# Optimization experiments

Hardware: AMD Instinct MI355X
Metric: run time of the kernel (lower is better)

Reference implementation:

```python
import jax, jax.numpy as jnp
import numpy as np

TEMPERATURE = 1.0
MIN_DISP = 0.1


def setup_inputs() -> dict:
    key = jax.random.key(0)
    k1, = jax.random.split(key, 1)
    B, V, C, H, W = 4, 2, 128, 128, 512
    feat = jax.random.normal(k1, (B, V, C, H, W), dtype=jnp.float32)
    # normalized intrinsics (fx < 50 triggers normalized_intri branch)
    K = jnp.array([[0.8, 0.0, 0.5], [0.0, 0.8, 0.5], [0.0, 0.0, 1.0]], dtype=jnp.float32)
    intri = jnp.broadcast_to(K, (B, V, 3, 3))
    # extrinsics: left = identity, right = identity translated by baseline 0.1 in x
    eye = jnp.eye(4, dtype=jnp.float32)
    lext = jnp.broadcast_to(eye, (B, 4, 4))
    rext = eye.at[0, 3].set(0.1)
    rext = jnp.broadcast_to(rext, (B, 4, 4))
    extri = jnp.stack([lext, rext], axis=1)
    near = jnp.full((B, V), 0.1, dtype=jnp.float32)
    far = jnp.full((B, V), 10.0, dtype=jnp.float32)
    return {"feat": feat, "extri": extri, "intri": intri, "near": near, "far": far}


def reference(feat, extri, intri, near, far):
    B, V, C, H, W = feat.shape
    lfeat, rfeat = feat[:, 0], feat[:, 1]          # (B,C,H,W)
    lintri = intri[:, 0]
    lextri, rextri = extri[:, 0], extri[:, 1]
    lfar = far[:, 0]

    # dot-product cost volume, groups G=1: (B,1,H,W1,W2)
    vol = jnp.einsum('bchi,bchj->bhij', lfeat, rfeat) / np.sqrt(C)
    vol = vol[:, None]

    # triangular geometry mask (left image first -> tril), applied AFTER softmax
    mask = jnp.tril(jnp.ones((W, W), dtype=vol.dtype))
    idx = jnp.arange(W, dtype=vol.dtype)
    prob = jax.nn.softmax(vol / TEMPERATURE, axis=-1) * mask

    # soft-argmax correspondence and confidence
    corresp = jnp.sum(prob * idx, axis=-1)         # (B,1,H,W)
    conf = jnp.max(prob, axis=-1)                  # (B,1,H,W)

    # correspondence -> normalized disparity -> depth
    disp = jnp.abs(corresp - idx) / W
    disp = jnp.maximum(disp, MIN_DISP)
    fx = lintri[:, 0, 0][:, None, None, None]
    baseline = jnp.linalg.norm(lextri[:, :3, 3] - rextri[:, :3, 3], axis=-1)
    depth = fx * baseline[:, None, None, None] / disp

    # depth_type == 'norm_depth'
    depth_conversed = depth / lfar[:, None, None, None]

    out = jnp.concatenate((depth_conversed, conf), axis=1)[:, None]  # (B,1,2,H,W)
    return out
```

## Files before the change

### kernel.cpp

```cpp
#include <hip/hip_runtime.h>

typedef _Float16 f16x8 __attribute__((ext_vector_type(8)));
typedef _Float16 f16x4 __attribute__((ext_vector_type(4)));
typedef float    f32x4 __attribute__((ext_vector_type(4)));

#define C_DIM 128
#define H_DIM 128
#define W_DIM 512
#define CH_STRIDE 65536
#define V_STRIDE  8388608
#define SJ 32
#define NSTRIP 16
#define ROW_H 136

__global__ __launch_bounds__(512, 2) void costvol_kernel(
    const float* __restrict__ feat,
    const float* __restrict__ extri,
    const float* __restrict__ intri,
    const float* __restrict__ farp,
    float* __restrict__ out)
{
    __shared__ _Float16 Bs[2][SJ][ROW_H];

    const int tid  = threadIdx.x;
    const int wave = tid >> 6;
    const int lane = tid & 63;
    const int l15  = lane & 15;
    const int l4   = lane >> 4;

    const int bh = blockIdx.x;
    const int b  = bh >> 7;
    const int h  = bh & 127;

    const float* lbase = feat + (size_t)(b * 2) * V_STRIDE + (size_t)h * W_DIM;
    const float* rbase = lbase + V_STRIDE;

    const int jj = tid & 31;
    const int c0 = (tid >> 5) * 4;

    float br[8];
    {
        const float* bp = rbase + jj;
        #pragma unroll
        for (int d = 0; d < 4; ++d) {
            br[d]     = bp[(size_t)(c0 + d) * CH_STRIDE];
            br[4 + d] = bp[(size_t)(c0 + d + 64) * CH_STRIDE];
        }
    }
    __builtin_amdgcn_sched_barrier(0);

    f16x8 a[4][4];
    const float kScale = 0.08838834764831845f;
    #pragma unroll
    for (int ks = 0; ks < 4; ++ks) {
        #pragma unroll
        for (int fi = 0; fi < 4; ++fi) {
            const float* p = lbase + (size_t)(ks * 32 + l4 * 8) * CH_STRIDE
                             + (size_t)(wave * 64 + fi * 16 + l15);
            f16x8 f;
            #pragma unroll
            for (int e = 0; e < 8; ++e)
                f[e] = (_Float16)(p[(size_t)e * CH_STRIDE] * kScale);
            a[fi][ks] = f;
        }
        __builtin_amdgcn_sched_barrier(0);
    }

    {
        f16x4 w0, w1;
        #pragma unroll
        for (int d = 0; d < 4; ++d) { w0[d] = (_Float16)br[d]; w1[d] = (_Float16)br[4 + d]; }
        *(f16x4*)&Bs[0][jj][c0]      = w0;
        *(f16x4*)&Bs[0][jj][c0 + 64] = w1;
    }
    __syncthreads();

    float Zp[16], Mp[16], Wp[16];
    #pragma unroll
    for (int s2 = 0; s2 < 16; ++s2) { Zp[s2] = 0.f; Mp[s2] = 0.f; Wp[s2] = 0.f; }

    int buf = 0;
    for (int s = 0; s < NSTRIP; ++s) {
        if (s + 1 < NSTRIP) {
            const float* bp = rbase + (size_t)((s + 1) * SJ + jj);
            #pragma unroll
            for (int d = 0; d < 4; ++d) {
                br[d]     = bp[(size_t)(c0 + d) * CH_STRIDE];
                br[4 + d] = bp[(size_t)(c0 + d + 64) * CH_STRIDE];
            }
        }
        __builtin_amdgcn_sched_barrier(0);

        f32x4 acc[4][2];
        #pragma unroll
        for (int fi = 0; fi < 4; ++fi) {
            acc[fi][0] = (f32x4){0.f, 0.f, 0.f, 0.f};
            acc[fi][1] = (f32x4){0.f, 0.f, 0.f, 0.f};
        }
        #pragma unroll
        for (int ks = 0; ks < 4; ++ks) {
            f16x8 b0 = *(const f16x8*)&Bs[buf][l15][ks * 32 + l4 * 8];
            f16x8 b1 = *(const f16x8*)&Bs[buf][16 + l15][ks * 32 + l4 * 8];
            #pragma unroll
            for (int fi = 0; fi < 4; ++fi) {
                acc[fi][0] = __builtin_amdgcn_mfma_f32_16x16x32_f16(a[fi][ks], b0, acc[fi][0], 0, 0, 0);
                acc[fi][1] = __builtin_amdgcn_mfma_f32_16x16x32_f16(a[fi][ks], b1, acc[fi][1], 0, 0, 0);
            }
        }

        const int jbase = s * SJ;
        #pragma unroll
        for (int fi = 0; fi < 4; ++fi) {
            const int ti0 = wave * 64 + fi * 16;
            #pragma unroll
            for (int fj = 0; fj < 2; ++fj) {
                const int tj = jbase + fj * 16;
                const float jf = (float)(tj + l15);
                if (tj + 15 <= ti0) {
                    #pragma unroll
                    for (int r = 0; r < 4; ++r) {
                        const int sl = fi * 4 + r;
                        float e = __expf(acc[fi][fj][r]);
                        Zp[sl] += e;
                        Mp[sl] = fmaxf(Mp[sl], e);
                        Wp[sl] += jf * e;
                    }
                } else if (tj > ti0 + 15) {
                    #pragma unroll
                    for (int r = 0; r < 4; ++r) {
                        float e = __expf(acc[fi][fj][r]);
                        Zp[fi * 4 + r] += e;
                    }
                } else {
                    #pragma unroll
                    for (int r = 0; r < 4; ++r) {
                        const int sl = fi * 4 + r;
                        float e = __expf(acc[fi][fj][r]);
                        Zp[sl] += e;
                        const int irow = ti0 + l4 * 4 + r;
                        float em = ((tj + l15) <= irow) ? e : 0.f;
                        Mp[sl] = fmaxf(Mp[sl], em);
                        Wp[sl] += jf * em;
                    }
                }
            }
        }

        if (s + 1 < NSTRIP) {
            f16x4 w0, w1;
            #pragma unroll
            for (int d = 0; d < 4; ++d) { w0[d] = (_Float16)br[d]; w1[d] = (_Float16)br[4 + d]; }
            *(f16x4*)&Bs[buf ^ 1][jj][c0]      = w0;
            *(f16x4*)&Bs[buf ^ 1][jj][c0 + 64] = w1;
        }
        __syncthreads();
        buf ^= 1;
    }

    #pragma unroll
    for (int m = 1; m <= 8; m <<= 1) {
        #pragma unroll
        for (int sl = 0; sl < 16; ++sl) {
            Zp[sl] += __shfl_xor(Zp[sl], m, 64);
            Wp[sl] += __shfl_xor(Wp[sl], m, 64);
            Mp[sl] = fmaxf(Mp[sl], __shfl_xor(Mp[sl], m, 64));
        }
    }

    if (l15 == 0) {
        const float fx = intri[b * 18];
        const float dx = extri[b * 32 + 3]  - extri[b * 32 + 19];
        const float dy = extri[b * 32 + 7]  - extri[b * 32 + 23];
        const float dz = extri[b * 32 + 11] - extri[b * 32 + 27];
        const float bl = sqrtf(dx * dx + dy * dy + dz * dz);
        const float lfar = farp[b * 2];
        const float kd = fx * bl / lfar;
        #pragma unroll
        for (int sl = 0; sl < 16; ++sl) {
            const int fi = sl >> 2, r = sl & 3;
            const int irow = wave * 64 + fi * 16 + l4 * 4 + r;
            const float Z = Zp[sl];
            const float conf = Mp[sl] / Z;
            const float corr = Wp[sl] / Z;
            float disp = fabsf(corr - (float)irow) * (1.0f / 512.0f);
            disp = fmaxf(disp, 0.1f);
            out[(size_t)(b * 2 + 0) * CH_STRIDE + h * W_DIM + irow] = kd / disp;
            out[(size_t)(b * 2 + 1) * CH_STRIDE + h * W_DIM + irow] = conf;
        }
    }
}

extern "C" void kernel_launch(void* const* d_in, const int* in_sizes, int n_in,
                              void* d_out, int out_size, void* d_ws, size_t ws_size,
                              hipStream_t stream) {
    const float* feat  = (const float*)d_in[0];
    const float* extri = (const float*)d_in[1];
    const float* intri = (const float*)d_in[2];
    const float* farp  = (const float*)d_in[4];
    float* out = (float*)d_out;
    costvol_kernel<<<dim3(512), dim3(512), 0, stream>>>(feat, extri, intri, farp, out);
}
```

Baseline: 90.92 us.

## Prefetch right-image strips two ahead with dual register buffers and MFMA priority

Restructures the strip loop to keep two register prefetch buffers in flight, so global loads for strip s+2 and s+3 overlap compute on earlier strips. Each thread now loads 8 consecutive channels and does one f16x8 LDS store instead of two f16x4 stores. It raises wave priority around the MFMA block and changes launch bounds to ask for 4 blocks per CU. The extra registers for the second buffer plus the tighter occupancy target risk spills or lower achieved occupancy.

```diff
diff --git a/kernel.cpp b/kernel.cpp
--- a/kernel.cpp
+++ b/kernel.cpp
@@ -1,7 +1,6 @@
 #include <hip/hip_runtime.h>
 
 typedef _Float16 f16x8 __attribute__((ext_vector_type(8)));
-typedef _Float16 f16x4 __attribute__((ext_vector_type(4)));
 typedef float    f32x4 __attribute__((ext_vector_type(4)));
 
 #define C_DIM 128
@@ -13,7 +12,7 @@
 #define NSTRIP 16
 #define ROW_H 136
 
-__global__ __launch_bounds__(512, 2) void costvol_kernel(
+__global__ __launch_bounds__(512, 4) void costvol_kernel(
     const float* __restrict__ feat,
     const float* __restrict__ extri,
     const float* __restrict__ intri,
@@ -36,17 +35,26 @@
     const float* rbase = lbase + V_STRIDE;
 
     const int jj = tid & 31;
-    const int c0 = (tid >> 5) * 4;
-
-    float br[8];
-    {
-        const float* bp = rbase + jj;
-        #pragma unroll
-        for (int d = 0; d < 4; ++d) {
-            br[d]     = bp[(size_t)(c0 + d) * CH_STRIDE];
-            br[4 + d] = bp[(size_t)(c0 + d + 64) * CH_STRIDE];
-        }
-    }
+    const int c0 = (tid >> 5) * 8;
+
+    float brA[8], brB[8];
+
+#define ISSUE(br, s) do {                                                   \
+    const float* bp_ = rbase + (size_t)((s) * SJ + jj);                     \
+    _Pragma("unroll")                                                       \
+    for (int d_ = 0; d_ < 8; ++d_)                                          \
+        (br)[d_] = bp_[(size_t)(c0 + d_) * CH_STRIDE];                      \
+} while (0)
+
+#define STAGE(br, bf) do {                                                  \
+    f16x8 w_;                                                               \
+    _Pragma("unroll")                                                       \
+    for (int d_ = 0; d_ < 8; ++d_) w_[d_] = (_Float16)(br)[d_];             \
+    *(f16x8*)&Bs[bf][jj][c0] = w_;                                          \
+} while (0)
+
+    ISSUE(brA, 0);
+    ISSUE(brB, 1);
     __builtin_amdgcn_sched_barrier(0);
 
     f16x8 a[4][4];
@@ -66,95 +74,84 @@
         __builtin_amdgcn_sched_barrier(0);
     }
 
-    {
-        f16x4 w0, w1;
-        #pragma unroll
-        for (int d = 0; d < 4; ++d) { w0[d] = (_Float16)br[d]; w1[d] = (_Float16)br[4 + d]; }
-        *(f16x4*)&Bs[0][jj][c0]      = w0;
-        *(f16x4*)&Bs[0][jj][c0 + 64] = w1;
-    }
+    STAGE(brA, 0);
     __syncthreads();
 
     float Zp[16], Mp[16], Wp[16];
     #pragma unroll
     for (int s2 = 0; s2 < 16; ++s2) { Zp[s2] = 0.f; Mp[s2] = 0.f; Wp[s2] = 0.f; }
 
-    int buf = 0;
-    for (int s = 0; s < NSTRIP; ++s) {
-        if (s + 1 < NSTRIP) {
-            const float* bp = rbase + (size_t)((s + 1) * SJ + jj);
-            #pragma unroll
-            for (int d = 0; d < 4; ++d) {
-                br[d]     = bp[(size_t)(c0 + d) * CH_STRIDE];
-                br[4 + d] = bp[(size_t)(c0 + d + 64) * CH_STRIDE];
-            }
-        }
+#define COMPUTE(bf, s) do {                                                  \
+    f32x4 acc[4][2];                                                         \
+    _Pragma("unroll")                                                        \
+    for (int fi = 0; fi < 4; ++fi) {                                         \
+        acc[fi][0] = (f32x4){0.f, 0.f, 0.f, 0.f};                            \
+        acc[fi][1] = (f32x4){0.f, 0.f, 0.f, 0.f};                            \
+    }                                                                        \
+    __builtin_amdgcn_s_setprio(1);                                           \
+    _Pragma("unroll")                                                        \
+    for (int ks = 0; ks < 4; ++ks) {                                         \
+        f16x8 b0 = *(const f16x8*)&Bs[bf][l15][ks * 32 + l4 * 8];            \
+        f16x8 b1 = *(const f16x8*)&Bs[bf][16 + l15][ks * 32 + l4 * 8];       \
+        _Pragma("unroll")                                                    \
+        for (int fi = 0; fi < 4; ++fi) {                                     \
+            acc[fi][0] = __builtin_amdgcn_mfma_f32_16x16x32_f16(a[fi][ks], b0, acc[fi][0], 0, 0, 0); \
+            acc[fi][1] = __builtin_amdgcn_mfma_f32_16x16x32_f16(a[fi][ks], b1, acc[fi][1], 0, 0, 0); \
+        }                                                                    \
+    }                                                                        \
+    __builtin_amdgcn_s_setprio(0);                                           \
+    const int jbase_ = (s) * SJ;                                             \
+    _Pragma("unroll")                                                        \
+    for (int fi = 0; fi < 4; ++fi) {                                         \
+        const int ti0 = wave * 64 + fi * 16;                                 \
+        _Pragma("unroll")                                                    \
+        for (int fj = 0; fj < 2; ++fj) {                                     \
+            const int tj = jbase_ + fj * 16;                                 \
+            const float jf = (float)(tj + l15);                              \
+            if (tj + 15 <= ti0) {                     \
+                _Pragma("unroll")                                            \
+                for (int r = 0; r < 4; ++r) {                                \
+                    const int sl = fi * 4 + r;                               \
+                    float e = __expf(acc[fi][fj][r]);                        \
+                    Zp[sl] += e;                                             \
+                    Mp[sl] = fmaxf(Mp[sl], e);                               \
+                    Wp[sl] += jf * e;                                        \
+                }                                                            \
+            } else if (tj > ti0 + 15) {                    \
+                _Pragma("unroll")                                            \
+                for (int r = 0; r < 4; ++r) {                                \
+                    float e = __expf(acc[fi][fj][r]);                        \
+                    Zp[fi * 4 + r] += e;                                     \
+                }                                                            \
+            } else {                                      \
+                _Pragma("unroll")                                            \
+                for (int r = 0; r < 4; ++r) {                                \
+                    const int sl = fi * 4 + r;                               \
+                    float e = __expf(acc[fi][fj][r]);                        \
+                    Zp[sl] += e;                                             \
+                    const int irow = ti0 + l4 * 4 + r;                       \
+                    float em = ((tj + l15) <= irow) ? e : 0.f;               \
+                    Mp[sl] = fmaxf(Mp[sl], em);                              \
+                    Wp[sl] += jf * em;                                       \
+                }                                                            \
+            }                                                                \
+        }                                                                    \
+    }                                                                        \
+} while (0)
+
+    #pragma unroll 1
+    for (int s = 0; s < NSTRIP; s += 2) {
+        if (s + 2 < NSTRIP) ISSUE(brA, s + 2);
         __builtin_amdgcn_sched_barrier(0);
-
-        f32x4 acc[4][2];
-        #pragma unroll
-        for (int fi = 0; fi < 4; ++fi) {
-            acc[fi][0] = (f32x4){0.f, 0.f, 0.f, 0.f};
-            acc[fi][1] = (f32x4){0.f, 0.f, 0.f, 0.f};
-        }
-        #pragma unroll
-        for (int ks = 0; ks < 4; ++ks) {
-            f16x8 b0 = *(const f16x8*)&Bs[buf][l15][ks * 32 + l4 * 8];
-            f16x8 b1 = *(const f16x8*)&Bs[buf][16 + l15][ks * 32 + l4 * 8];
-            #pragma unroll
-            for (int fi = 0; fi < 4; ++fi) {
-                acc[fi][0] = __builtin_amdgcn_mfma_f32_16x16x32_f16(a[fi][ks], b0, acc[fi][0], 0, 0, 0);
-                acc[fi][1] = __builtin_amdgcn_mfma_f32_16x16x32_f16(a[fi][ks], b1, acc[fi][1], 0, 0, 0);
-            }
-        }
-
-        const int jbase = s * SJ;
-        #pragma unroll
-        for (int fi = 0; fi < 4; ++fi) {
-            const int ti0 = wave * 64 + fi * 16;
-            #pragma unroll
-            for (int fj = 0; fj < 2; ++fj) {
-                const int tj = jbase + fj * 16;
-                const float jf = (float)(tj + l15);
-                if (tj + 15 <= ti0) {
-                    #pragma unroll
-                    for (int r = 0; r < 4; ++r) {
-                        const int sl = fi * 4 + r;
-                        float e = __expf(acc[fi][fj][r]);
-                        Zp[sl] += e;
-                        Mp[sl] = fmaxf(Mp[sl], e);
-                        Wp[sl] += jf * e;
-                    }
-                } else if (tj > ti0 + 15) {
-                    #pragma unroll
-                    for (int r = 0; r < 4; ++r) {
-                        float e = __expf(acc[fi][fj][r]);
-                        Zp[fi * 4 + r] += e;
-                    }
-                } else {
-                    #pragma unroll
-                    for (int r = 0; r < 4; ++r) {
-                        const int sl = fi * 4 + r;
-                        float e = __expf(acc[fi][fj][r]);
-                        Zp[sl] += e;
-                        const int irow = ti0 + l4 * 4 + r;
-                        float em = ((tj + l15) <= irow) ? e : 0.f;
-                        Mp[sl] = fmaxf(Mp[sl], em);
-                        Wp[sl] += jf * em;
-                    }
-                }
-            }
-        }
-
-        if (s + 1 < NSTRIP) {
-            f16x4 w0, w1;
-            #pragma unroll
-            for (int d = 0; d < 4; ++d) { w0[d] = (_Float16)br[d]; w1[d] = (_Float16)br[4 + d]; }
-            *(f16x4*)&Bs[buf ^ 1][jj][c0]      = w0;
-            *(f16x4*)&Bs[buf ^ 1][jj][c0 + 64] = w1;
-        }
+        COMPUTE(0, s);
+        STAGE(brB, 1);
         __syncthreads();
-        buf ^= 1;
+
+        if (s + 3 < NSTRIP) ISSUE(brB, s + 3);
+        __builtin_amdgcn_sched_barrier(0);
+        COMPUTE(1, s + 1);
+        if (s + 2 < NSTRIP) STAGE(brA, 0);
+        __syncthreads();
     }
 
     #pragma unroll
@@ -188,6 +185,9 @@
             out[(size_t)(b * 2 + 1) * CH_STRIDE + h * W_DIM + irow] = conf;
         }
     }
+#undef ISSUE
+#undef STAGE
+#undef COMPUTE
 }
 
 extern "C" void kernel_launch(void* const* d_in, const int* in_sizes, int n_in,
```

After: 328.8 us. 262% more time.

## Stage full right row in LDS, use 1024-thread blocks and exp2

Applied to the files above, without the earlier changes.

The kernel now loads the entire right-image row (512 columns × 128 channels, fp16) into LDS in one pass instead of double-buffering 32-column strips. This removes the per-strip barriers and the pipelined global prefetch. Blocks grow to 16 waves, each owning 32 rows, with the MFMA phase at raised wave priority. The log2(e) factor is folded into the A scaling so exp2f can replace expf. In exchange, the single upfront load is no longer overlapped with compute, and the larger LDS footprint (~139KB) may cap occupancy at one block per CU despite the launch-bounds hint.

```diff
diff --git a/kernel.cpp b/kernel.cpp
--- a/kernel.cpp
+++ b/kernel.cpp
@@ -1,7 +1,6 @@
 #include <hip/hip_runtime.h>
 
 typedef _Float16 f16x8 __attribute__((ext_vector_type(8)));
-typedef _Float16 f16x4 __attribute__((ext_vector_type(4)));
 typedef float    f32x4 __attribute__((ext_vector_type(4)));
 
 #define C_DIM 128
@@ -9,18 +8,16 @@
 #define W_DIM 512
 #define CH_STRIDE 65536
 #define V_STRIDE  8388608
-#define SJ 32
-#define NSTRIP 16
 #define ROW_H 136
 
-__global__ __launch_bounds__(512, 2) void costvol_kernel(
+__global__ __launch_bounds__(1024, 4) void costvol_kernel(
     const float* __restrict__ feat,
     const float* __restrict__ extri,
     const float* __restrict__ intri,
     const float* __restrict__ farp,
     float* __restrict__ out)
 {
-    __shared__ _Float16 Bs[2][SJ][ROW_H];
+    __shared__ _Float16 Bs[W_DIM][ROW_H];
 
     const int tid  = threadIdx.x;
     const int wave = tid >> 6;
@@ -31,136 +28,100 @@
     const int bh = blockIdx.x;
     const int b  = bh >> 7;
     const int h  = bh & 127;
+    const int rowbase = wave * 32;
 
     const float* lbase = feat + (size_t)(b * 2) * V_STRIDE + (size_t)h * W_DIM;
     const float* rbase = lbase + V_STRIDE;
 
-    const int jj = tid & 31;
-    const int c0 = (tid >> 5) * 4;
-
-    float br[8];
-    {
-        const float* bp = rbase + jj;
-        #pragma unroll
-        for (int d = 0; d < 4; ++d) {
-            br[d]     = bp[(size_t)(c0 + d) * CH_STRIDE];
-            br[4 + d] = bp[(size_t)(c0 + d + 64) * CH_STRIDE];
-        }
-    }
-    __builtin_amdgcn_sched_barrier(0);
-
-    f16x8 a[4][4];
-    const float kScale = 0.08838834764831845f;
+    f16x8 a[2][4];
+    const float kScale = 0.08838834764831845f * 1.44269504088896340f;
     #pragma unroll
     for (int ks = 0; ks < 4; ++ks) {
         #pragma unroll
-        for (int fi = 0; fi < 4; ++fi) {
+        for (int fi = 0; fi < 2; ++fi) {
             const float* p = lbase + (size_t)(ks * 32 + l4 * 8) * CH_STRIDE
-                             + (size_t)(wave * 64 + fi * 16 + l15);
+                             + (size_t)(rowbase + fi * 16 + l15);
             f16x8 f;
             #pragma unroll
             for (int e = 0; e < 8; ++e)
                 f[e] = (_Float16)(p[(size_t)e * CH_STRIDE] * kScale);
             a[fi][ks] = f;
         }
-        __builtin_amdgcn_sched_barrier(0);
     }
 
     {
-        f16x4 w0, w1;
+        const int j      = tid & 511;
+        const int chbase = (tid >> 9) << 6;
         #pragma unroll
-        for (int d = 0; d < 4; ++d) { w0[d] = (_Float16)br[d]; w1[d] = (_Float16)br[4 + d]; }
-        *(f16x4*)&Bs[0][jj][c0]      = w0;
-        *(f16x4*)&Bs[0][jj][c0 + 64] = w1;
+        for (int cb = 0; cb < 8; ++cb) {
+            const int c0 = chbase + cb * 8;
+            const float* bp = rbase + (size_t)c0 * CH_STRIDE + j;
+            f16x8 w;
+            #pragma unroll
+            for (int e = 0; e < 8; ++e)
+                w[e] = (_Float16)bp[(size_t)e * CH_STRIDE];
+            *(f16x8*)&Bs[j][c0] = w;
+        }
     }
     __syncthreads();
 
-    float Zp[16], Mp[16], Wp[16];
+    float Zp[8], Mp[8], Wp[8];
     #pragma unroll
-    for (int s2 = 0; s2 < 16; ++s2) { Zp[s2] = 0.f; Mp[s2] = 0.f; Wp[s2] = 0.f; }
+    for (int s2 = 0; s2 < 8; ++s2) { Zp[s2] = 0.f; Mp[s2] = 0.f; Wp[s2] = 0.f; }
 
-    int buf = 0;
-    for (int s = 0; s < NSTRIP; ++s) {
-        if (s + 1 < NSTRIP) {
-            const float* bp = rbase + (size_t)((s + 1) * SJ + jj);
-            #pragma unroll
-            for (int d = 0; d < 4; ++d) {
-                br[d]     = bp[(size_t)(c0 + d) * CH_STRIDE];
-                br[4 + d] = bp[(size_t)(c0 + d + 64) * CH_STRIDE];
-            }
-        }
-        __builtin_amdgcn_sched_barrier(0);
-
-        f32x4 acc[4][2];
-        #pragma unroll
-        for (int fi = 0; fi < 4; ++fi) {
-            acc[fi][0] = (f32x4){0.f, 0.f, 0.f, 0.f};
-            acc[fi][1] = (f32x4){0.f, 0.f, 0.f, 0.f};
-        }
+    #pragma unroll 1
+    for (int jt = 0; jt < 32; ++jt) {
+        f32x4 acc[2];
+        acc[0] = (f32x4){0.f, 0.f, 0.f, 0.f};
+        acc[1] = (f32x4){0.f, 0.f, 0.f, 0.f};
+        __builtin_amdgcn_s_setprio(1);
         #pragma unroll
         for (int ks = 0; ks < 4; ++ks) {
-            f16x8 b0 = *(const f16x8*)&Bs[buf][l15][ks * 32 + l4 * 8];
-            f16x8 b1 = *(const f16x8*)&Bs[buf][16 + l15][ks * 32 + l4 * 8];
-            #pragma unroll
-            for (int fi = 0; fi < 4; ++fi) {
-                acc[fi][0] = __builtin_amdgcn_mfma_f32_16x16x32_f16(a[fi][ks], b0, acc[fi][0], 0, 0, 0);
-                acc[fi][1] = __builtin_amdgcn_mfma_f32_16x16x32_f16(a[fi][ks], b1, acc[fi][1], 0, 0, 0);
-            }
+            f16x8 bf = *(const f16x8*)&Bs[jt * 16 + l15][ks * 32 + l4 * 8];
+            acc[0] = __builtin_amdgcn_mfma_f32_16x16x32_f16(a[0][ks], bf, acc[0], 0, 0, 0);
+            acc[1] = __builtin_amdgcn_mfma_f32_16x16x32_f16(a[1][ks], bf, acc[1], 0, 0, 0);
         }
+        __builtin_amdgcn_s_setprio(0);
 
-        const int jbase = s * SJ;
+        const int tj = jt * 16;
+        const float jf = (float)(tj + l15);
         #pragma unroll
-        for (int fi = 0; fi < 4; ++fi) {
-            const int ti0 = wave * 64 + fi * 16;
-            #pragma unroll
-            for (int fj = 0; fj < 2; ++fj) {
-                const int tj = jbase + fj * 16;
-                const float jf = (float)(tj + l15);
-                if (tj + 15 <= ti0) {
-                    #pragma unroll
-                    for (int r = 0; r < 4; ++r) {
-                        const int sl = fi * 4 + r;
-                        float e = __expf(acc[fi][fj][r]);
-                        Zp[sl] += e;
-                        Mp[sl] = fmaxf(Mp[sl], e);
-                        Wp[sl] += jf * e;
-                    }
-                } else if (tj > ti0 + 15) {
-                    #pragma unroll
-                    for (int r = 0; r < 4; ++r) {
-                        float e = __expf(acc[fi][fj][r]);
-                        Zp[fi * 4 + r] += e;
-                    }
-                } else {
-                    #pragma unroll
-                    for (int r = 0; r < 4; ++r) {
-                        const int sl = fi * 4 + r;
-                        float e = __expf(acc[fi][fj][r]);
-                        Zp[sl] += e;
-                        const int irow = ti0 + l4 * 4 + r;
-                        float em = ((tj + l15) <= irow) ? e : 0.f;
-                        Mp[sl] = fmaxf(Mp[sl], em);
-                        Wp[sl] += jf * em;
-                    }
+        for (int fi = 0; fi < 2; ++fi) {
+            const int ti0 = rowbase + fi * 16;
+            if (tj + 15 <= ti0) {
+                #pragma unroll
+                for (int r = 0; r < 4; ++r) {
+                    const int sl = fi * 4 + r;
+                    float e = exp2f(acc[fi][r]);
+                    Zp[sl] += e;
+                    Mp[sl] = fmaxf(Mp[sl], e);
+                    Wp[sl] += jf * e;
+                }
+            } else if (tj > ti0 + 15) {
+                #pragma unroll
+                for (int r = 0; r < 4; ++r) {
+                    float e = exp2f(acc[fi][r]);
+                    Zp[fi * 4 + r] += e;
+                }
+            } else {
+                #pragma unroll
+                for (int r = 0; r < 4; ++r) {
+                    const int sl = fi * 4 + r;
+                    float e = exp2f(acc[fi][r]);
+                    Zp[sl] += e;
+                    const int irow = ti0 + l4 * 4 + r;
+                    float em = ((tj + l15) <= irow) ? e : 0.f;
+                    Mp[sl] = fmaxf(Mp[sl], em);
+                    Wp[sl] += jf * em;
                 }
             }
         }
-
-        if (s + 1 < NSTRIP) {
-            f16x4 w0, w1;
-            #pragma unroll
-            for (int d = 0; d < 4; ++d) { w0[d] = (_Float16)br[d]; w1[d] = (_Float16)br[4 + d]; }
-            *(f16x4*)&Bs[buf ^ 1][jj][c0]      = w0;
-            *(f16x4*)&Bs[buf ^ 1][jj][c0 + 64] = w1;
-        }
-        __syncthreads();
-        buf ^= 1;
     }
 
     #pragma unroll
     for (int m = 1; m <= 8; m <<= 1) {
         #pragma unroll
-        for (int sl = 0; sl < 16; ++sl) {
+        for (int sl = 0; sl < 8; ++sl) {
             Zp[sl] += __shfl_xor(Zp[sl], m, 64);
             Wp[sl] += __shfl_xor(Wp[sl], m, 64);
             Mp[sl] = fmaxf(Mp[sl], __shfl_xor(Mp[sl], m, 64));
@@ -176,9 +137,9 @@
         const float lfar = farp[b * 2];
         const float kd = fx * bl / lfar;
         #pragma unroll
-        for (int sl = 0; sl < 16; ++sl) {
+        for (int sl = 0; sl < 8; ++sl) {
             const int fi = sl >> 2, r = sl & 3;
-            const int irow = wave * 64 + fi * 16 + l4 * 4 + r;
+            const int irow = rowbase + fi * 16 + l4 * 4 + r;
             const float Z = Zp[sl];
             const float conf = Mp[sl] / Z;
             const float corr = Wp[sl] / Z;
@@ -198,5 +159,5 @@
     const float* intri = (const float*)d_in[2];
     const float* farp  = (const float*)d_in[4];
     float* out = (float*)d_out;
-    costvol_kernel<<<dim3(512), dim3(512), 0, stream>>>(feat, extri, intri, farp, out);
+    costvol_kernel<<<dim3(512), dim3(1024), 0, stream>>>(feat, extri, intri, farp, out);
 }
```

Result: slower. 99.56 us (+9.5%).
